# Performance work log

Measured on AMD Instinct MI355X. Metric: run time of the kernel, lower is better.

The kernel has to match this reference:

```python
import jax, jax.numpy as jnp
import numpy as np

B, T, S, H, C, E, V, OOV = 8, 16, 400, 512, 512, 128, 50000, 50


def setup_inputs() -> dict:
    key = jax.random.key(0)
    ks = jax.random.split(key, 24)
    rn = lambda k, shape, s=0.05: jax.random.normal(k, shape, dtype=jnp.float32) * s
    inp = {
        'input_embeddings': rn(ks[0], (B, T, E), 1.0),
        'context': rn(ks[1], (B, 1, C), 1.0),
        'h0': rn(ks[2], (1, B, H), 1.0),
        'c0': rn(ks[3], (1, B, H), 1.0),
        'encoder_outputs': rn(ks[4], (B, S, C), 1.0),
        'encoder_masks': jnp.ones((B, S), jnp.float32),
        'extra_zeros': jnp.zeros((B, OOV), jnp.float32),
        'extended_source_idx': jax.random.randint(ks[5], (B, S), 0, V + OOV),
        'coverage': jnp.zeros((B, 1, S), jnp.float32),
        # LSTM (single layer), torch gate order i,f,g,o
        'W_ih': rn(ks[6], (4 * H, E)), 'W_hh': rn(ks[7], (4 * H, H)),
        'b_ih': rn(ks[8], (4 * H,)), 'b_hh': rn(ks[9], (4 * H,)),
        # attention (concat + coverage)
        'cov_w': rn(ks[10], (H, 1)),
        'energy_w': rn(ks[11], (H, H + C)), 'energy_b': rn(ks[12], (H,)),
        'v': jax.random.uniform(ks[13], (H,), jnp.float32),
        # projections
        'xctx_w': rn(ks[14], (E, E + C)), 'xctx_b': rn(ks[15], (E,)),
        'attnd_w': rn(ks[16], (H, H + C)), 'attnd_b': rn(ks[17], (H,)),
        'vocab_w': rn(ks[18], (V, H)), 'vocab_b': rn(ks[19], (V,)),
        'pgen_w': rn(ks[20], (1, C + H + E)), 'pgen_b': rn(ks[21], (1,)),
    }
    return inp


def reference(input_embeddings, context, h0, c0, encoder_outputs, encoder_masks,
              extra_zeros, extended_source_idx, coverage,
              W_ih, W_hh, b_ih, b_hh, cov_w, energy_w, energy_b, v,
              xctx_w, xctx_b, attnd_w, attnd_b, vocab_w, vocab_b, pgen_w, pgen_b):
    Bn = input_embeddings.shape[0]
    Sn = encoder_outputs.shape[1]
    bidx = jnp.arange(Bn)[:, None]

    def step(carry, emb_t):
        h, c, ctx, cov = carry  # [B,H],[B,H],[B,C],[B,S]
        x = jnp.concatenate([emb_t, ctx], -1) @ xctx_w.T + xctx_b  # [B,E]
        gates = x @ W_ih.T + b_ih + h @ W_hh.T + b_hh
        i, f, g, o = jnp.split(gates, 4, axis=-1)
        c_new = jax.nn.sigmoid(f) * c + jax.nn.sigmoid(i) * jnp.tanh(g)
        h_new = jax.nn.sigmoid(o) * jnp.tanh(c_new)  # [B,H]
        # concat-style Luong attention with coverage
        cov_proj = cov[..., None] * cov_w[:, 0]  # [B,S,H] (Linear(1,H) no bias)
        cat = jnp.concatenate([
            jnp.broadcast_to(h_new[:, None, :], (Bn, Sn, h_new.shape[-1])),
            encoder_outputs], -1)  # [B,S,H+C]
        energy = jnp.tanh(cat @ energy_w.T + energy_b + cov_proj)
        e = energy @ v  # [B,S]
        probs = jax.nn.softmax(e, -1) * encoder_masks
        probs = probs / (probs.sum(-1, keepdims=True) + 1e-12)
        ctx_new = jnp.einsum('bs,bsc->bc', probs, encoder_outputs)
        cov_new = cov + probs
        vocab_dist = jax.nn.softmax(
            (jnp.concatenate([h_new, ctx_new], -1) @ attnd_w.T + attnd_b) @ vocab_w.T + vocab_b, -1)
        p_gen = jax.nn.sigmoid(jnp.concatenate([ctx_new, h_new, x], -1) @ pgen_w.T + pgen_b)  # [B,1]
        ext = jnp.concatenate([vocab_dist * p_gen, extra_zeros], 1)  # [B,V+OOV]
        final = ext.at[bidx, extended_source_idx].add((1.0 - p_gen) * probs)
        return (h_new, c_new, ctx_new, cov_new), (final, probs, cov_new, p_gen)

    init = (h0[0], c0[0], context[:, 0], coverage[:, 0])
    (h, c, ctx, cov), (finals, attns, covs, pgens) = jax.lax.scan(
        step, init, jnp.swapaxes(input_embeddings, 0, 1))
    final_vocab_dists = jnp.swapaxes(finals, 0, 1)  # [B,T,V+OOV]
    attn_dists = jnp.swapaxes(attns, 0, 1)          # [B,T,S]
    coverages = jnp.swapaxes(covs, 0, 1)            # [B,T,S]
    return (final_vocab_dists, ctx[:, None, :], h[None], c[None], attn_dists, pgens[-1], coverages)
```

## Files before the change

### kernel.cpp

```cpp
#include <hip/hip_runtime.h>
#include <math.h>

#define BB 8
#define TT 16
#define SS 400
#define HH 512
#define EE 128
#define VV 50000
#define VE 50050
#define OOVn 50

#define O1 6406400
#define O2 6410496
#define O3 6414592
#define O4 6418688
#define O5 6469888
#define O6 6469896

#define G_OFF    0
#define EWHB_OFF 1179648
#define ENCP_OFF 4600000
#define PM_OFF   5700000
#define CTXR_OFF 5800000

typedef __attribute__((ext_vector_type(4))) float floatx4;
typedef __attribute__((ext_vector_type(8))) short short8;
typedef __attribute__((ext_vector_type(8))) unsigned short ushort8_t;
typedef __attribute__((ext_vector_type(4))) unsigned short ushort4_t;

__device__ __forceinline__ float sigm(float x){ return 1.0f/(1.0f+__expf(-x)); }
__device__ __forceinline__ float ftanh(float x){
  float e = __expf(2.0f*x); return 1.0f - 2.0f/(e + 1.0f);
}
__device__ __forceinline__ unsigned short f2bf(float f){
  union { float f; unsigned int u; } v; v.f = f;
  unsigned int u = v.u;
  return (unsigned short)((u + 0x7FFFu + ((u >> 16) & 1u)) >> 16);
}
__device__ __forceinline__ float bfu(unsigned short u){
  union { unsigned int i; float f; } v; v.i = ((unsigned int)u) << 16; return v.f;
}

__global__ __launch_bounds__(256)
void gemm_bt(const float* __restrict__ A, int lda,
             const float* __restrict__ Bm, int ldb,
             const float* __restrict__ bias,
             float* __restrict__ Cm, int ldc,
             int N, int K, int permute, int obf,
             long bsB, long bsC)
{
  __shared__ unsigned short Ash[128*72];
  __shared__ unsigned short Bsh[64*72];
  int tid = threadIdx.x;
  int mbase = blockIdx.x * 128;
  int nbase = blockIdx.y * 64;
  long z = blockIdx.z;
  const float* Bz = Bm + z*bsB;
  int wave = tid >> 6, lane = tid & 63;
  int wm = (wave & 1) * 64, wn = (wave >> 1) * 32;
  int fl = lane & 15, quad = lane >> 4;

  floatx4 acc[4][2];
  for (int i=0;i<4;i++) for(int j=0;j<2;j++) acc[i][j] = (floatx4)(0.0f);

  for (int kc = 0; kc < K; kc += 64) {
    float4 ra[8], rb[4];
#pragma unroll
    for (int i = 0; i < 8; ++i) {
      int idx = tid + i*256;
      int row = idx >> 4;
      int c4 = (idx & 15) << 2;
      ra[i] = *(const float4*)(A + (size_t)(mbase+row)*lda + kc + c4);
    }
#pragma unroll
    for (int i = 0; i < 4; ++i) {
      int idx = tid + i*256;
      int row = idx >> 4;
      int c4 = (idx & 15) << 2;
      int gn = nbase + row;
      if (gn < N) rb[i] = *(const float4*)(Bz + (size_t)gn*ldb + kc + c4);
      else { rb[i].x = 0.f; rb[i].y = 0.f; rb[i].z = 0.f; rb[i].w = 0.f; }
    }
    __syncthreads();
#pragma unroll
    for (int i = 0; i < 8; ++i) {
      int idx = tid + i*256;
      int o = (idx >> 4)*72 + ((idx & 15) << 2);
      Ash[o+0]=f2bf(ra[i].x); Ash[o+1]=f2bf(ra[i].y); Ash[o+2]=f2bf(ra[i].z); Ash[o+3]=f2bf(ra[i].w);
    }
#pragma unroll
    for (int i = 0; i < 4; ++i) {
      int idx = tid + i*256;
      int o = (idx >> 4)*72 + ((idx & 15) << 2);
      Bsh[o+0]=f2bf(rb[i].x); Bsh[o+1]=f2bf(rb[i].y); Bsh[o+2]=f2bf(rb[i].z); Bsh[o+3]=f2bf(rb[i].w);
    }
    __syncthreads();
#pragma unroll
    for (int ks = 0; ks < 2; ++ks) {
      short8 af[4], bfr[2];
      int ko = ks*32 + quad*8;
#pragma unroll
      for (int i=0;i<4;i++) af[i]  = *(const short8*)&Ash[(wm + i*16 + fl)*72 + ko];
#pragma unroll
      for (int j=0;j<2;j++) bfr[j] = *(const short8*)&Bsh[(wn + j*16 + fl)*72 + ko];
#pragma unroll
      for (int i=0;i<4;i++)
#pragma unroll
        for (int j=0;j<2;j++)
          acc[i][j] = __builtin_amdgcn_mfma_f32_16x16x32_bf16(af[i], bfr[j], acc[i][j], 0,0,0);
    }
    __syncthreads();
  }
  for (int i=0;i<4;i++){
    for (int j=0;j<2;j++){
      int nc = nbase + wn + j*16 + fl;
      if (nc >= N) continue;
      float bv = bias ? bias[nc] : 0.0f;
      for (int r=0;r<4;r++){
        int mg = mbase + wm + i*16 + quad*4 + r;
        int orow = permute ? ((mg & 7)*16 + (mg >> 3)) : mg;
        float v = acc[i][j][r] + bv;
        long ci = (long)orow*ldc + nc + z*bsC;
        if (obf) ((unsigned short*)Cm)[ci] = f2bf(v);
        else     Cm[ci] = v;
      }
    }
  }
}

__global__ __launch_bounds__(256)
void gemm_logits(const unsigned short* __restrict__ Abf,
                 const float* __restrict__ Bm, const float* __restrict__ bias,
                 float* __restrict__ out, float* __restrict__ rowsum)
{
  __shared__ unsigned short Ash[128*72];
  __shared__ unsigned short Bsh[64*72];
  __shared__ float rowpart[128];
  int tid = threadIdx.x;
  int nbase = blockIdx.x * 64;
  int wave = tid >> 6, lane = tid & 63;
  int wm = (wave & 1) * 64, wn = (wave >> 1) * 32;
  int fl = lane & 15, quad = lane >> 4;

  floatx4 acc[4][2];
  for (int i=0;i<4;i++) for(int j=0;j<2;j++) acc[i][j] = (floatx4)(0.0f);
  if (tid < 128) rowpart[tid] = 0.f;

  for (int kc = 0; kc < 512; kc += 64) {
    ushort8_t raa[4];
    float4 rb[4];
#pragma unroll
    for (int i = 0; i < 4; ++i) {
      int idx = tid + i*256;
      int row = idx >> 3;
      int c8 = (idx & 7) << 3;
      raa[i] = *(const ushort8_t*)(Abf + (size_t)row*512 + kc + c8);
    }
#pragma unroll
    for (int i = 0; i < 4; ++i) {
      int idx = tid + i*256;
      int row = idx >> 4;
      int c4 = (idx & 15) << 2;
      int gn = nbase + row;
      if (gn < VV) rb[i] = *(const float4*)(Bm + (size_t)gn*512 + kc + c4);
      else { rb[i].x = 0.f; rb[i].y = 0.f; rb[i].z = 0.f; rb[i].w = 0.f; }
    }
    __syncthreads();
#pragma unroll
    for (int i = 0; i < 4; ++i) {
      int idx = tid + i*256;
      int o = (idx >> 3)*72 + ((idx & 7) << 3);
      *(ushort8_t*)&Ash[o] = raa[i];
    }
#pragma unroll
    for (int i = 0; i < 4; ++i) {
      int idx = tid + i*256;
      int o = (idx >> 4)*72 + ((idx & 15) << 2);
      Bsh[o+0]=f2bf(rb[i].x); Bsh[o+1]=f2bf(rb[i].y); Bsh[o+2]=f2bf(rb[i].z); Bsh[o+3]=f2bf(rb[i].w);
    }
    __syncthreads();
#pragma unroll
    for (int ks = 0; ks < 2; ++ks) {
      short8 af[4], bfr[2];
      int ko = ks*32 + quad*8;
#pragma unroll
      for (int i=0;i<4;i++) af[i]  = *(const short8*)&Ash[(wm + i*16 + fl)*72 + ko];
#pragma unroll
      for (int j=0;j<2;j++) bfr[j] = *(const short8*)&Bsh[(wn + j*16 + fl)*72 + ko];
#pragma unroll
      for (int i=0;i<4;i++)
#pragma unroll
        for (int j=0;j<2;j++)
          acc[i][j] = __builtin_amdgcn_mfma_f32_16x16x32_bf16(af[i], bfr[j], acc[i][j], 0,0,0);
    }
    __syncthreads();
  }
  for (int i=0;i<4;i++){
    for (int r=0;r<4;r++){
      int mg = wm + i*16 + quad*4 + r;
      int orow = (mg & 7)*16 + (mg >> 3);
      float rs = 0.f;
      for (int j=0;j<2;j++){
        int nc = nbase + wn + j*16 + fl;
        if (nc < VV) {
          float e = __expf(acc[i][j][r] + bias[nc]);
          out[(size_t)orow*VE + nc] = e;
          rs += e;
        }
      }
      atomicAdd(&rowpart[mg], rs);
    }
  }
  __syncthreads();
  if (tid < 128) {
    int orow = (tid & 7)*16 + (tid >> 3);
    atomicAdd(&rowsum[orow], rowpart[tid]);
  }
}

__global__ __launch_bounds__(256) void p_wx(const float* __restrict__ wih,
    const float* __restrict__ whh, const float* __restrict__ xcw,
    unsigned short* __restrict__ G)
{
  int blk = blockIdx.x, tid = threadIdx.x;
  if (blk < 640) {
    int rt = blk / 10, ct = blk % 10;
    __shared__ float wl[32*128];
    __shared__ float xl[128*64];
    for (int i = tid; i < 4096; i += 256) {
      int r = i >> 7, k = i & 127;
      wl[i] = wih[(size_t)(rt*32+r)*128 + k];
    }
    for (int i = tid; i < 8192; i += 256) {
      int e = i >> 6, c = i & 63;
      xl[i] = xcw[(size_t)e*640 + ct*64 + c];
    }
    __syncthreads();
    for (int o = tid; o < 2048; o += 256) {
      int r = o >> 6, c = o & 63;
      float acc = 0.f;
      for (int e = 0; e < 128; ++e) acc += wl[r*128+e]*xl[e*64+c];
      G[(size_t)(rt*32+r)*1152 + ct*64 + c] = f2bf(acc);
    }
  } else {
    int idx = blk - 640;
    for (int q = 0; q < 2; ++q) {
      int n = idx*2048 + q*1024 + tid*4;
      int r = n >> 9, k = n & 511;
      float4 v = *(const float4*)(whh + n);
      ushort4_t s; s[0]=f2bf(v.x); s[1]=f2bf(v.y); s[2]=f2bf(v.z); s[3]=f2bf(v.w);
      *(ushort4_t*)(G + (size_t)r*1152 + 640 + k) = s;
    }
  }
}

__global__ __launch_bounds__(256) void p_small(const float* __restrict__ wih,
    const float* __restrict__ bih, const float* __restrict__ bhh,
    const float* __restrict__ xb, const float* __restrict__ xcw,
    const float* __restrict__ pw, const float* __restrict__ pb,
    float* __restrict__ gb, float* __restrict__ q, float* __restrict__ qb,
    float* __restrict__ d1, float* __restrict__ d2)
{
  int blk = blockIdx.x, tid = threadIdx.x;
  if (blk < 8) {
    __shared__ float xbl[128];
    if (tid < 128) xbl[tid] = xb[tid];
    __syncthreads();
    int r = blk*256 + tid;
    const float* wr = wih + (size_t)r*128;
    float acc = bih[r] + bhh[r];
    for (int e = 0; e < 128; ++e) acc += wr[e]*xbl[e];
    gb[r] = acc;
  } else if (blk < 11) {
    int o = (blk-8)*256 + tid;
    if (o < 640) {
      float acc = 0.f;
      for (int e = 0; e < 128; ++e) acc += pw[1024+e]*xcw[(size_t)e*640 + o];
      q[o] = acc;
    }
  } else {
    if (tid == 0) {
      float acc = 0.f;
      for (int e = 0; e < 128; ++e) acc += pw[1024+e]*xb[e];
      qb[0] = acc + pb[0];
    }
    if (tid < 128) { d1[tid] = 0.f; d2[tid] = 0.f; }
  }
}

__global__ __launch_bounds__(256) void p_cast(const float* __restrict__ ew,
    unsigned short* __restrict__ ewhb, float* __restrict__ ctxraw)
{
  int blk = blockIdx.x, tid = threadIdx.x;
  for (int q = 0; q < 2; ++q) {
    size_t n = (size_t)blk*2048 + q*1024 + tid*4;
    int p = (int)(n >> 9), k = (int)(n & 511);
    float4 v = *(const float4*)(ew + (size_t)p*1024 + k);
    ushort4_t s; s[0]=f2bf(v.x); s[1]=f2bf(v.y); s[2]=f2bf(v.z); s[3]=f2bf(v.w);
    *(ushort4_t*)(ewhb + n) = s;
  }
  for (int i = tid; i < 512; i += 256) ctxraw[(size_t)blk*512 + i] = 0.f;
}

__global__ __launch_bounds__(256) void s1g(
    const unsigned short* __restrict__ G,
    const float* __restrict__ gb,
    const float* __restrict__ emb, const float* __restrict__ context,
    const float* __restrict__ h0, const float* __restrict__ c0,
    const float* __restrict__ coverage,
    const float* __restrict__ PM, const float* __restrict__ d1,
    const float* __restrict__ d2, const float* __restrict__ ctxraw,
    float* __restrict__ A1, float* __restrict__ c_cur,
    float* __restrict__ out, int t)
{
  __shared__ float ueh[8][644];
  __shared__ float uc[8][516];
  __shared__ float part[256];
  __shared__ float gl[64];
  __shared__ float invs[8];
  int tid = threadIdx.x, blk = blockIdx.x;

  if (t >= 1 && tid < 8)
    invs[tid] = 1.0f / (d2[(t-1)*8 + tid] + 1e-12f*d1[(t-1)*8 + tid]);
  __syncthreads();

  for (int i = 0; i < 5; ++i) {
    int slot = i*256 + tid;
    int b = slot / 160, sl = slot - b*160;
    if (sl < 32) {
      *(float4*)&ueh[b][sl*4] = *(const float4*)(emb + (size_t)(b*16+t)*128 + sl*4);
    } else {
      int qq = sl - 32;
      const float* hsrc = t ? (A1 + ((size_t)((t-1)*8+b))*1024) : (h0 + b*512);
      *(float4*)&ueh[b][128 + qq*4] = *(const float4*)(hsrc + qq*4);
    }
  }
  for (int i = 0; i < 4; ++i) {
    int slot = i*256 + tid;
    int b = slot >> 7, sl = slot & 127;
    const float* csrc = t ? (ctxraw + ((size_t)((t-1)*8+b))*512)
                          : (context + (size_t)b*512);
    float4 v = *(const float4*)(csrc + sl*4);
    if (t) { float iv = invs[b]; v.x*=iv; v.y*=iv; v.z*=iv; v.w*=iv; }
    *(float4*)&uc[b][sl*4] = v;
  }
  __syncthreads();

  if (t >= 1 && blk < 8) {
    int b = blk;
    float iv = invs[b];
    const float* covprev = (t == 1) ? (coverage + b*400)
                                    : (out + O6 + ((size_t)(b*16 + t-2))*400);
    const float* pmsrc = PM + (size_t)(t-1)*3200 + b*400;
    size_t o = ((size_t)(b*16 + t-1))*400;
    for (int s = tid; s < 400; s += 256) {
      float pr = pmsrc[s] * iv;
      out[O4 + o + s] = pr;
      out[O6 + o + s] = covprev[s] + pr;
    }
  }

  int dot = tid >> 2, kq = tid & 3;
  int rr = dot >> 3, b = dot & 7;
  int gate = rr >> 1, jj = rr & 1;
  int r = gate*512 + blk*2 + jj;
  const unsigned short* gr = G + (size_t)r*1152;
  float acc = 0.f;
  {
    const unsigned short* gp = gr + kq*8;
    const float* up = &ueh[b][kq*8];
#pragma unroll
    for (int i = 0; i < 4; ++i) {
      ushort8_t w8 = *(const ushort8_t*)(gp + i*32);
      float4 u0 = *(const float4*)(up + i*32);
      float4 u1 = *(const float4*)(up + i*32 + 4);
      acc += bfu(w8[0])*u0.x + bfu(w8[1])*u0.y + bfu(w8[2])*u0.z + bfu(w8[3])*u0.w
           + bfu(w8[4])*u1.x + bfu(w8[5])*u1.y + bfu(w8[6])*u1.z + bfu(w8[7])*u1.w;
    }
  }
  {
    const unsigned short* gp = gr + 128 + kq*8;
    const float* up = &uc[b][kq*8];
#pragma unroll 4
    for (int i = 0; i < 16; ++i) {
      ushort8_t w8 = *(const ushort8_t*)(gp + i*32);
      float4 u0 = *(const float4*)(up + i*32);
      float4 u1 = *(const float4*)(up + i*32 + 4);
      acc += bfu(w8[0])*u0.x + bfu(w8[1])*u0.y + bfu(w8[2])*u0.z + bfu(w8[3])*u0.w
           + bfu(w8[4])*u1.x + bfu(w8[5])*u1.y + bfu(w8[6])*u1.z + bfu(w8[7])*u1.w;
    }
  }
  {
    const unsigned short* gp = gr + 640 + kq*8;
    const float* up = &ueh[b][128 + kq*8];
#pragma unroll 4
    for (int i = 0; i < 16; ++i) {
      ushort8_t w8 = *(const ushort8_t*)(gp + i*32);
      float4 u0 = *(const float4*)(up + i*32);
      float4 u1 = *(const float4*)(up + i*32 + 4);
      acc += bfu(w8[0])*u0.x + bfu(w8[1])*u0.y + bfu(w8[2])*u0.z + bfu(w8[3])*u0.w
           + bfu(w8[4])*u1.x + bfu(w8[5])*u1.y + bfu(w8[6])*u1.z + bfu(w8[7])*u1.w;
    }
  }
  part[tid] = acc;
  __syncthreads();
  if (tid < 64) {
    int rr2 = tid >> 3;
    int r2 = (rr2 >> 1)*512 + blk*2 + (rr2 & 1);
    gl[tid] = part[tid*4] + part[tid*4+1] + part[tid*4+2] + part[tid*4+3] + gb[r2];
  }
  __syncthreads();
  if (tid < 16) {
    int jj2 = tid >> 3, b2 = tid & 7;
    float gi = gl[(0*2+jj2)*8 + b2];
    float gf = gl[(1*2+jj2)*8 + b2];
    float gg = gl[(2*2+jj2)*8 + b2];
    float go = gl[(3*2+jj2)*8 + b2];
    int j = blk*2 + jj2;
    float cp = t ? c_cur[b2*512+j] : c0[b2*512+j];
    float cn = sigm(gf)*cp + sigm(gi)*ftanh(gg);
    float hn = sigm(go)*ftanh(cn);
    c_cur[b2*512+j] = cn;
    A1[((size_t)(t*8+b2))*1024 + j] = hn;
  }
}

__global__ __launch_bounds__(256) void s2_hp(
    const unsigned short* __restrict__ ewhb, const float* __restrict__ eb,
    const float* __restrict__ A1, float* __restrict__ hp, int t)
{
  __shared__ float hl[8*516];
  __shared__ float part[256];
  int tid = threadIdx.x, pc = blockIdx.x;
  for (int b = 0; b < 8; ++b)
    for (int k = tid; k < 512; k += 256)
      hl[b*516 + k] = A1[((size_t)(t*8+b))*1024 + k];
  __syncthreads();
  int dot = tid >> 2, kq = tid & 3;
  int rr = dot >> 3, b = dot & 7;
  int p = pc*8 + rr;
  const unsigned short* wp = ewhb + (size_t)p*512 + kq*16;
  const float* hh = hl + b*516 + kq*16;
  float acc = 0.f;
#pragma unroll
  for (int i = 0; i < 8; ++i) {
    ushort8_t wa = *(const ushort8_t*)(wp + i*64);
    ushort8_t wb = *(const ushort8_t*)(wp + i*64 + 8);
    float4 h0v = *(const float4*)(hh + i*64);
    float4 h1v = *(const float4*)(hh + i*64 + 4);
    float4 h2v = *(const float4*)(hh + i*64 + 8);
    float4 h3v = *(const float4*)(hh + i*64 + 12);
    acc += bfu(wa[0])*h0v.x + bfu(wa[1])*h0v.y + bfu(wa[2])*h0v.z + bfu(wa[3])*h0v.w
         + bfu(wa[4])*h1v.x + bfu(wa[5])*h1v.y + bfu(wa[6])*h1v.z + bfu(wa[7])*h1v.w
         + bfu(wb[0])*h2v.x + bfu(wb[1])*h2v.y + bfu(wb[2])*h2v.z + bfu(wb[3])*h2v.w
         + bfu(wb[4])*h3v.x + bfu(wb[5])*h3v.y + bfu(wb[6])*h3v.z + bfu(wb[7])*h3v.w;
  }
  part[tid] = acc;
  __syncthreads();
  if (tid < 64) {
    int rr2 = tid >> 3, b2 = tid & 7;
    int p2 = pc*8 + rr2;
    hp[b2*512 + p2] = eb[p2] + part[tid*4] + part[tid*4+1] + part[tid*4+2] + part[tid*4+3];
  }
}

__global__ __launch_bounds__(256) void s3e(
    const unsigned short* __restrict__ encpb, const float* __restrict__ hp,
    const float* __restrict__ vvec, const float* __restrict__ covw,
    const float* __restrict__ masks, const float* __restrict__ coverage,
    const float* __restrict__ out6v, const float* __restrict__ enc,
    float* __restrict__ PM, float* __restrict__ d1, float* __restrict__ d2,
    float* __restrict__ ctxraw, int t)
{
  int tid = threadIdx.x;
  int b = blockIdx.x >> 4, sc = blockIdx.x & 15;
  int w = tid >> 6, lane = tid & 63;
  int h0i = lane*8;
  __shared__ float red1[4], red2[4];
  __shared__ float pms[25];
  float hpv[8], vv[8], cw[8];
  {
    const float* hpp = hp + b*512 + h0i;
    float4 a0 = *(const float4*)(hpp), a1 = *(const float4*)(hpp+4);
    hpv[0]=a0.x; hpv[1]=a0.y; hpv[2]=a0.z; hpv[3]=a0.w;
    hpv[4]=a1.x; hpv[5]=a1.y; hpv[6]=a1.z; hpv[7]=a1.w;
    float4 v0 = *(const float4*)(vvec+h0i), v1 = *(const float4*)(vvec+h0i+4);
    vv[0]=v0.x; vv[1]=v0.y; vv[2]=v0.z; vv[3]=v0.w;
    vv[4]=v1.x; vv[5]=v1.y; vv[6]=v1.z; vv[7]=v1.w;
    float4 c0v = *(const float4*)(covw+h0i), c1v = *(const float4*)(covw+h0i+4);
    cw[0]=c0v.x; cw[1]=c0v.y; cw[2]=c0v.z; cw[3]=c0v.w;
    cw[4]=c1v.x; cw[5]=c1v.y; cw[6]=c1v.z; cw[7]=c1v.w;
  }
  const float* covp = t ? (out6v + ((size_t)(b*16 + t-1))*400) : (coverage + b*400);
  float a1s = 0.f, a2s = 0.f;
  for (int sl = w; sl < 25; sl += 4) {
    int s = sc*25 + sl;
    float cv = covp[s];
    const unsigned short* ep = encpb + ((size_t)(b*400+s))*512 + h0i;
    ushort8_t e8 = *(const ushort8_t*)ep;
    float acc = 0.f;
#pragma unroll
    for (int i = 0; i < 8; ++i)
      acc += ftanh(hpv[i] + bfu(e8[i]) + cv*cw[i]) * vv[i];
    for (int off = 32; off > 0; off >>= 1) acc += __shfl_down(acc, off);
    if (lane == 0) {
      float pe = __expf(acc);
      float pmv = pe * masks[b*400 + s];
      PM[(size_t)t*3200 + b*400 + s] = pmv;
      pms[sl] = pmv;
      a1s += pe; a2s += pmv;
    }
  }
  if (lane == 0) { red1[w] = a1s; red2[w] = a2s; }
  __syncthreads();
  if (tid == 0) {
    atomicAdd(&d1[t*8+b], red1[0]+red1[1]+red1[2]+red1[3]);
    atomicAdd(&d2[t*8+b], red2[0]+red2[1]+red2[2]+red2[3]);
  }
  {
    float acc0 = 0.f, acc1 = 0.f;
    const float* encb = enc + ((size_t)(b*400 + sc*25))*512;
#pragma unroll 5
    for (int sl = 0; sl < 25; ++sl) {
      float pmv = pms[sl];
      const float* er = encb + (size_t)sl*512;
      acc0 += pmv * er[tid];
      acc1 += pmv * er[tid + 256];
    }
    float* cr = ctxraw + ((size_t)(t*8+b))*512;
    atomicAdd(&cr[tid], acc0);
    atomicAdd(&cr[tid+256], acc1);
  }
}

__global__ __launch_bounds__(256) void e_pgen(
    const float* __restrict__ A1f, const float* __restrict__ c_cur,
    const float* __restrict__ emb, const float* __restrict__ context,
    const float* __restrict__ pw, const float* __restrict__ q,
    const float* __restrict__ qb,
    const float* __restrict__ d1, const float* __restrict__ d2,
    const float* __restrict__ ctxraw, const float* __restrict__ PM,
    float* __restrict__ A1, float* __restrict__ pgen,
    float* __restrict__ rowsum, float* __restrict__ out)
{
  int blk = blockIdx.x, tid = threadIdx.x;
  if (blk < 128) {
    int m = blk, t = m >> 3, b = m & 7;
    __shared__ float invT, invP;
    if (tid == 0) invT = 1.0f / (d2[m] + 1e-12f*d1[m]);
    if (tid == 64) invP = t ? 1.0f / (d2[m-8] + 1e-12f*d1[m-8]) : 0.f;
    __syncthreads();
    const float* crT = ctxraw + (size_t)m*512;
    const float* crP = ctxraw + (size_t)(t ? m-8 : m)*512;
    const float* hT   = A1f + (size_t)m*1024;
    const float* embp = emb + (size_t)(b*16+t)*128;
    float acc = 0.f;
    for (int k = tid; k < 512; k += 256) {
      float cT = crT[k] * invT;
      float cP = t ? crP[k] * invP : context[(size_t)b*512 + k];
      acc += pw[k]*cT + pw[512+k]*hT[k] + q[128+k]*cP;
      A1[(size_t)m*1024 + 512 + k] = cT;
    }
    if (tid < 128) acc += q[tid]*embp[tid];
    for (int off = 32; off > 0; off >>= 1) acc += __shfl_down(acc, off);
    __shared__ float red[4];
    if (!(tid & 63)) red[tid>>6] = acc;
    __syncthreads();
    if (tid == 0) {
      float pg = sigm(red[0]+red[1]+red[2]+red[3] + qb[0]);
      pgen[m] = pg;
      if (t == 15) out[O5 + b] = pg;
    }
  } else if (blk == 128) {
    for (int i = tid; i < 4096; i += 256) {
      int b = i >> 9, j = i & 511;
      float inv = 1.0f / (d2[120+b] + 1e-12f*d1[120+b]);
      out[O1 + i] = ctxraw[(size_t)(120+b)*512 + j] * inv;
    }
  } else if (blk == 129) {
    for (int i = tid; i < 4096; i += 256) {
      int b = i >> 9, j = i & 511;
      out[O2 + i] = A1f[((size_t)(120+b))*1024 + j];
    }
  } else if (blk == 130) {
    for (int i = tid; i < 4096; i += 256) out[O3 + i] = c_cur[i];
  } else if (blk == 131) {
    if (tid < 128) rowsum[tid] = 0.f;
  } else {
    int b = blk - 132;
    float inv = 1.0f / (d2[120+b] + 1e-12f*d1[120+b]);
    const float* pmsrc = PM + (size_t)15*3200 + b*400;
    size_t o15 = ((size_t)(b*16 + 15))*400;
    size_t o14 = ((size_t)(b*16 + 14))*400;
    for (int s = tid; s < 400; s += 256) {
      float pr = pmsrc[s] * inv;
      out[O4 + o15 + s] = pr;
      out[O6 + o15 + s] = out[O6 + o14 + s] + pr;
    }
  }
}

__global__ __launch_bounds__(256) void k_scale(
    float* __restrict__ out, const float* __restrict__ pgen,
    const float* __restrict__ rowsum, const float* __restrict__ ez)
{
  int orow = blockIdx.x, cy = blockIdx.y, tid = threadIdx.x;
  int b = orow >> 4, t = orow & 15;
  float sc = pgen[t*8+b] / rowsum[orow];
  int c0 = cy*6256;
  int c1 = (cy == 7) ? VE : c0 + 6256;
  float* row = out + (size_t)orow*VE;
  for (int c = c0 + tid*4; c < c1; c += 1024) {
    if (c + 4 <= VV && c + 4 <= c1) {
      float4 v = *(float4*)(row + c);
      v.x *= sc; v.y *= sc; v.z *= sc; v.w *= sc;
      *(float4*)(row + c) = v;
    } else {
      for (int e = 0; e < 4; ++e) {
        int cc2 = c + e;
        if (cc2 < c1) row[cc2] = (cc2 < VV) ? row[cc2]*sc : ez[b*OOVn + cc2 - VV];
      }
    }
  }
}

__global__ __launch_bounds__(256) void k_scatter(
    float* __restrict__ out, const float* __restrict__ pgen,
    const int* __restrict__ extidx)
{
  int m = blockIdx.x, tid = threadIdx.x;
  int b = m & 7, t = m >> 3;
  float* row = out + ((size_t)(b*TT + t))*VE;
  float onem = 1.0f - pgen[m];
  const float* pr = out + O4 + ((size_t)(b*TT+t))*SS;
  for (int s = tid; s < SS; s += 256) {
    int ix = extidx[b*SS + s];
    atomicAdd(&row[ix], onem * pr[s]);
  }
}

extern "C" void kernel_launch(void* const* d_in, const int* in_sizes, int n_in,
                              void* d_out, int out_size, void* d_ws, size_t ws_size,
                              hipStream_t stream)
{
  (void)in_sizes; (void)n_in; (void)out_size; (void)ws_size;
  const float* emb      = (const float*)d_in[0];
  const float* context  = (const float*)d_in[1];
  const float* h0       = (const float*)d_in[2];
  const float* c0       = (const float*)d_in[3];
  const float* enc      = (const float*)d_in[4];
  const float* masks    = (const float*)d_in[5];
  const float* ez       = (const float*)d_in[6];
  const int*   extidx   = (const int*)d_in[7];
  const float* coverage = (const float*)d_in[8];
  const float* wih      = (const float*)d_in[9];
  const float* whh      = (const float*)d_in[10];
  const float* bih      = (const float*)d_in[11];
  const float* bhh      = (const float*)d_in[12];
  const float* covw     = (const float*)d_in[13];
  const float* ew       = (const float*)d_in[14];
  const float* eb       = (const float*)d_in[15];
  const float* vvec     = (const float*)d_in[16];
  const float* xw       = (const float*)d_in[17];
  const float* xb       = (const float*)d_in[18];
  const float* aw       = (const float*)d_in[19];
  const float* ab       = (const float*)d_in[20];
  const float* vw       = (const float*)d_in[21];
  const float* vb       = (const float*)d_in[22];
  const float* pw       = (const float*)d_in[23];
  const float* pb       = (const float*)d_in[24];
  float* out = (float*)d_out;

  float* ws = (float*)d_ws;
  float* A1       = ws;
  float* c_cur    = ws + 131072;
  float* hp       = ws + 135168;
  unsigned short* attnd_bf = (unsigned short*)(ws + 139264);
  float* pgen     = ws + 172032;
  float* gb       = ws + 172160;
  float* q        = ws + 174208;
  float* qb       = ws + 174848;
  float* d1       = ws + 174852;
  float* d2       = ws + 174980;
  float* rowsum   = ws + 175108;

  unsigned short* G     = (unsigned short*)(out + G_OFF);
  unsigned short* ewhb  = (unsigned short*)(out + EWHB_OFF);
  unsigned short* encpb = (unsigned short*)(out + ENCP_OFF);
  float*          PM    = out + PM_OFF;
  float*          ctxr  = out + CTXR_OFF;

  p_wx<<<1152, 256, 0, stream>>>(wih, whh, xw, G);
  p_small<<<12, 256, 0, stream>>>(wih, bih, bhh, xb, xw, pw, pb, gb, q, qb, d1, d2);
  p_cast<<<128, 256, 0, stream>>>(ew, ewhb, ctxr);
  gemm_bt<<<dim3(25,8,1), 256, 0, stream>>>(enc, 512, ew + 512, 1024,
      (const float*)nullptr, (float*)encpb, 512, 512, 512, 0, 1, 0, 0);

  for (int t = 0; t < TT; ++t) {
    s1g<<<256, 256, 0, stream>>>(G, gb, emb, context, h0, c0, coverage,
                                 PM, d1, d2, ctxr, A1, c_cur, out, t);
    s2_hp<<<64, 256, 0, stream>>>(ewhb, eb, A1, hp, t);
    s3e<<<128, 256, 0, stream>>>(encpb, hp, vvec, covw, masks, coverage,
                                 out + O6, enc, PM, d1, d2, ctxr, t);
  }

  e_pgen<<<140, 256, 0, stream>>>(A1, c_cur, emb, context, pw, q, qb,
                                  d1, d2, ctxr, PM, A1, pgen, rowsum, out);
  gemm_bt<<<dim3(1,8,1), 256, 0, stream>>>(A1, 1024, aw, 1024, ab,
      (float*)attnd_bf, 512, 512, 1024, 0, 1, 0, 0);
  gemm_logits<<<782, 256, 0, stream>>>(attnd_bf, vw, vb, out, rowsum);
  k_scale<<<dim3(128,8), 256, 0, stream>>>(out, pgen, rowsum, ez);
  k_scatter<<<128, 256, 0, stream>>>(out, pgen, extidx);
}
```

Before: 771.9 us.

## Fuse hidden-state energy projection into attention kernel, dropping per-step launch

Removes the separate s2_hp kernel that computed the hidden-state part of the attention energy, hp = energy_w_h·h + b. Each s3e block now recomputes the full 512-row projection for its own batch row, using a wave shuffle reduction, and keeps the result in shared memory. This cuts one kernel launch and one global round trip per timestep, 16 in total. In exchange, the 16 blocks that share a batch row each redo the same 512x512 bf16 matvec, so weight reads and compute go up 16x for that stage.

Result: slower. 796.7 us (+3.2%).

```diff
diff --git a/kernel.cpp b/kernel.cpp
--- a/kernel.cpp
+++ b/kernel.cpp
@@ -39,6 +39,13 @@
 }
 __device__ __forceinline__ float bfu(unsigned short u){
   union { unsigned int i; float f; } v; v.i = ((unsigned int)u) << 16; return v.f;
+}
+__device__ __forceinline__ float mac8(const unsigned short* w, const float* u) {
+  ushort8_t w8 = *(const ushort8_t*)w;
+  float4 u0 = *(const float4*)u;
+  float4 u1 = *(const float4*)(u+4);
+  return bfu(w8[0])*u0.x + bfu(w8[1])*u0.y + bfu(w8[2])*u0.z + bfu(w8[3])*u0.w
+       + bfu(w8[4])*u1.x + bfu(w8[5])*u1.y + bfu(w8[6])*u1.z + bfu(w8[7])*u1.w;
 }
 
 __global__ __launch_bounds__(256)
@@ -370,37 +377,19 @@
     const unsigned short* gp = gr + kq*8;
     const float* up = &ueh[b][kq*8];
 #pragma unroll
-    for (int i = 0; i < 4; ++i) {
-      ushort8_t w8 = *(const ushort8_t*)(gp + i*32);
-      float4 u0 = *(const float4*)(up + i*32);
-      float4 u1 = *(const float4*)(up + i*32 + 4);
-      acc += bfu(w8[0])*u0.x + bfu(w8[1])*u0.y + bfu(w8[2])*u0.z + bfu(w8[3])*u0.w
-           + bfu(w8[4])*u1.x + bfu(w8[5])*u1.y + bfu(w8[6])*u1.z + bfu(w8[7])*u1.w;
-    }
+    for (int i = 0; i < 4; ++i) acc += mac8(gp + i*32, up + i*32);
   }
   {
     const unsigned short* gp = gr + 128 + kq*8;
     const float* up = &uc[b][kq*8];
 #pragma unroll 4
-    for (int i = 0; i < 16; ++i) {
-      ushort8_t w8 = *(const ushort8_t*)(gp + i*32);
-      float4 u0 = *(const float4*)(up + i*32);
-      float4 u1 = *(const float4*)(up + i*32 + 4);
-      acc += bfu(w8[0])*u0.x + bfu(w8[1])*u0.y + bfu(w8[2])*u0.z + bfu(w8[3])*u0.w
-           + bfu(w8[4])*u1.x + bfu(w8[5])*u1.y + bfu(w8[6])*u1.z + bfu(w8[7])*u1.w;
-    }
+    for (int i = 0; i < 16; ++i) acc += mac8(gp + i*32, up + i*32);
   }
   {
     const unsigned short* gp = gr + 640 + kq*8;
     const float* up = &ueh[b][128 + kq*8];
 #pragma unroll 4
-    for (int i = 0; i < 16; ++i) {
-      ushort8_t w8 = *(const ushort8_t*)(gp + i*32);
-      float4 u0 = *(const float4*)(up + i*32);
-      float4 u1 = *(const float4*)(up + i*32 + 4);
-      acc += bfu(w8[0])*u0.x + bfu(w8[1])*u0.y + bfu(w8[2])*u0.z + bfu(w8[3])*u0.w
-           + bfu(w8[4])*u1.x + bfu(w8[5])*u1.y + bfu(w8[6])*u1.z + bfu(w8[7])*u1.w;
-    }
+    for (int i = 0; i < 16; ++i) acc += mac8(gp + i*32, up + i*32);
   }
   part[tid] = acc;
   __syncthreads();
@@ -425,47 +414,10 @@
   }
 }
 
-__global__ __launch_bounds__(256) void s2_hp(
-    const unsigned short* __restrict__ ewhb, const float* __restrict__ eb,
-    const float* __restrict__ A1, float* __restrict__ hp, int t)
-{
-  __shared__ float hl[8*516];
-  __shared__ float part[256];
-  int tid = threadIdx.x, pc = blockIdx.x;
-  for (int b = 0; b < 8; ++b)
-    for (int k = tid; k < 512; k += 256)
-      hl[b*516 + k] = A1[((size_t)(t*8+b))*1024 + k];
-  __syncthreads();
-  int dot = tid >> 2, kq = tid & 3;
-  int rr = dot >> 3, b = dot & 7;
-  int p = pc*8 + rr;
-  const unsigned short* wp = ewhb + (size_t)p*512 + kq*16;
-  const float* hh = hl + b*516 + kq*16;
-  float acc = 0.f;
-#pragma unroll
-  for (int i = 0; i < 8; ++i) {
-    ushort8_t wa = *(const ushort8_t*)(wp + i*64);
-    ushort8_t wb = *(const ushort8_t*)(wp + i*64 + 8);
-    float4 h0v = *(const float4*)(hh + i*64);
-    float4 h1v = *(const float4*)(hh + i*64 + 4);
-    float4 h2v = *(const float4*)(hh + i*64 + 8);
-    float4 h3v = *(const float4*)(hh + i*64 + 12);
-    acc += bfu(wa[0])*h0v.x + bfu(wa[1])*h0v.y + bfu(wa[2])*h0v.z + bfu(wa[3])*h0v.w
-         + bfu(wa[4])*h1v.x + bfu(wa[5])*h1v.y + bfu(wa[6])*h1v.z + bfu(wa[7])*h1v.w
-         + bfu(wb[0])*h2v.x + bfu(wb[1])*h2v.y + bfu(wb[2])*h2v.z + bfu(wb[3])*h2v.w
-         + bfu(wb[4])*h3v.x + bfu(wb[5])*h3v.y + bfu(wb[6])*h3v.z + bfu(wb[7])*h3v.w;
-  }
-  part[tid] = acc;
-  __syncthreads();
-  if (tid < 64) {
-    int rr2 = tid >> 3, b2 = tid & 7;
-    int p2 = pc*8 + rr2;
-    hp[b2*512 + p2] = eb[p2] + part[tid*4] + part[tid*4+1] + part[tid*4+2] + part[tid*4+3];
-  }
-}
-
 __global__ __launch_bounds__(256) void s3e(
-    const unsigned short* __restrict__ encpb, const float* __restrict__ hp,
+    const unsigned short* __restrict__ encpb,
+    const unsigned short* __restrict__ ewhb,
+    const float* __restrict__ eb, const float* __restrict__ A1,
     const float* __restrict__ vvec, const float* __restrict__ covw,
     const float* __restrict__ masks, const float* __restrict__ coverage,
     const float* __restrict__ out6v, const float* __restrict__ enc,
@@ -474,16 +426,41 @@
 {
   int tid = threadIdx.x;
   int b = blockIdx.x >> 4, sc = blockIdx.x & 15;
+  __shared__ float hl[512];
+  __shared__ float hpl[512];
+  __shared__ float red1[4], red2[4];
+  __shared__ float pms[25];
+
+  if (tid < 128)
+    *(float4*)&hl[tid*4] = *(const float4*)(A1 + ((size_t)(t*8+b))*1024 + tid*4);
+  __syncthreads();
+
+  {
+    int dot = tid >> 2, kq = tid & 3;
+    const float* hh = hl + kq*16;
+#pragma unroll
+    for (int pass = 0; pass < 8; ++pass) {
+      int p = pass*64 + dot;
+      const unsigned short* wp = ewhb + (size_t)p*512 + kq*16;
+      float acc = 0.f;
+#pragma unroll
+      for (int i = 0; i < 8; ++i) {
+        acc += mac8(wp + i*64, hh + i*64);
+        acc += mac8(wp + i*64 + 8, hh + i*64 + 8);
+      }
+      acc += __shfl_down(acc, 1);
+      acc += __shfl_down(acc, 2);
+      if (kq == 0) hpl[p] = eb[p] + acc;
+    }
+  }
+  __syncthreads();
+
   int w = tid >> 6, lane = tid & 63;
   int h0i = lane*8;
-  __shared__ float red1[4], red2[4];
-  __shared__ float pms[25];
   float hpv[8], vv[8], cw[8];
   {
-    const float* hpp = hp + b*512 + h0i;
-    float4 a0 = *(const float4*)(hpp), a1 = *(const float4*)(hpp+4);
-    hpv[0]=a0.x; hpv[1]=a0.y; hpv[2]=a0.z; hpv[3]=a0.w;
-    hpv[4]=a1.x; hpv[5]=a1.y; hpv[6]=a1.z; hpv[7]=a1.w;
+#pragma unroll
+    for (int i = 0; i < 8; ++i) hpv[i] = hpl[h0i + i];
     float4 v0 = *(const float4*)(vvec+h0i), v1 = *(const float4*)(vvec+h0i+4);
     vv[0]=v0.x; vv[1]=v0.y; vv[2]=v0.z; vv[3]=v0.w;
     vv[4]=v1.x; vv[5]=v1.y; vv[6]=v1.z; vv[7]=v1.w;
@@ -674,7 +651,6 @@
   float* ws = (float*)d_ws;
   float* A1       = ws;
   float* c_cur    = ws + 131072;
-  float* hp       = ws + 135168;
   unsigned short* attnd_bf = (unsigned short*)(ws + 139264);
   float* pgen     = ws + 172032;
   float* gb       = ws + 172160;
@@ -699,9 +675,8 @@
   for (int t = 0; t < TT; ++t) {
     s1g<<<256, 256, 0, stream>>>(G, gb, emb, context, h0, c0, coverage,
                                  PM, d1, d2, ctxr, A1, c_cur, out, t);
-    s2_hp<<<64, 256, 0, stream>>>(ewhb, eb, A1, hp, t);
-    s3e<<<128, 256, 0, stream>>>(encpb, hp, vvec, covw, masks, coverage,
-                                 out + O6, enc, PM, d1, d2, ctxr, t);
+    s3e<<<128, 256, 0, stream>>>(encpb, ewhb, eb, A1, vvec, covw, masks,
+                                 coverage, out + O6, enc, PM, d1, d2, ctxr, t);
   }
 
   e_pgen<<<140, 256, 0, stream>>>(A1, c_cur, emb, context, pw, q, qb,
```

## Replace 8-block attnd GEMM with wide GEMV kernel and fuse scatter into scale

Applied to the files above, without the earlier changes.

The attnd projection weights are now cast to bf16 in the existing prep cast kernel. The 8-block tiled GEMM is replaced with a 1024-block GEMV-style kernel in which each block reduces 8 output features for 8 rows, so a previously badly underfilled launch spreads across the GPU. The pointer-generator scatter is folded into the scale kernel: each column slice adds its own in-range indices after scaling, which removes one launch. The costs are an extra weight-cast pass and each scale block rereading the attention probabilities and indices.

Result: faster. 746.2 us (-3.3%).

```diff
diff --git a/kernel.cpp b/kernel.cpp
--- a/kernel.cpp
+++ b/kernel.cpp
@@ -19,6 +19,7 @@
 
 #define G_OFF    0
 #define EWHB_OFF 1179648
+#define AWBF_OFF 1310720
 #define ENCP_OFF 4600000
 #define PM_OFF   5700000
 #define CTXR_OFF 5800000
@@ -39,6 +40,13 @@
 }
 __device__ __forceinline__ float bfu(unsigned short u){
   union { unsigned int i; float f; } v; v.i = ((unsigned int)u) << 16; return v.f;
+}
+__device__ __forceinline__ float mac8(const unsigned short* w, const float* u) {
+  ushort8_t w8 = *(const ushort8_t*)w;
+  float4 u0 = *(const float4*)u;
+  float4 u1 = *(const float4*)(u+4);
+  return bfu(w8[0])*u0.x + bfu(w8[1])*u0.y + bfu(w8[2])*u0.z + bfu(w8[3])*u0.w
+       + bfu(w8[4])*u1.x + bfu(w8[5])*u1.y + bfu(w8[6])*u1.z + bfu(w8[7])*u1.w;
 }
 
 __global__ __launch_bounds__(256)
@@ -218,6 +226,41 @@
   }
 }
 
+__global__ __launch_bounds__(256) void vk_attnd(
+    const float* __restrict__ A1, const unsigned short* __restrict__ awbf,
+    const float* __restrict__ ab, unsigned short* __restrict__ attnd_bf)
+{
+  __shared__ float hl[8][1032];
+  __shared__ float part[256];
+  int tid = threadIdx.x;
+  int pc = blockIdx.x & 63;
+  int mg = blockIdx.x >> 6;
+  int m0 = mg*8;
+#pragma unroll
+  for (int i = 0; i < 8; ++i)
+    *(float4*)&hl[i][tid*4] = *(const float4*)(A1 + (size_t)(m0+i)*1024 + tid*4);
+  __syncthreads();
+  int dot = tid >> 2, kq = tid & 3;
+  int lp = dot >> 3, lm = dot & 7;
+  int p = pc*8 + lp;
+  const unsigned short* wp = awbf + (size_t)p*1024 + kq*16;
+  const float* hh = &hl[lm][kq*16];
+  float acc = 0.f;
+#pragma unroll
+  for (int i = 0; i < 16; ++i) {
+    acc += mac8(wp + i*64, hh + i*64);
+    acc += mac8(wp + i*64 + 8, hh + i*64 + 8);
+  }
+  part[tid] = acc;
+  __syncthreads();
+  if (tid < 64) {
+    int lp2 = tid >> 3, lm2 = tid & 7;
+    int p2 = pc*8 + lp2;
+    float v = ab[p2] + part[tid*4] + part[tid*4+1] + part[tid*4+2] + part[tid*4+3];
+    attnd_bf[(size_t)(m0+lm2)*512 + p2] = f2bf(v);
+  }
+}
+
 __global__ __launch_bounds__(256) void p_wx(const float* __restrict__ wih,
     const float* __restrict__ whh, const float* __restrict__ xcw,
     unsigned short* __restrict__ G)
@@ -289,17 +332,28 @@
 }
 
 __global__ __launch_bounds__(256) void p_cast(const float* __restrict__ ew,
-    unsigned short* __restrict__ ewhb, float* __restrict__ ctxraw)
+    unsigned short* __restrict__ ewhb, const float* __restrict__ aw,
+    unsigned short* __restrict__ awbf, float* __restrict__ ctxraw)
 {
   int blk = blockIdx.x, tid = threadIdx.x;
-  for (int q = 0; q < 2; ++q) {
-    size_t n = (size_t)blk*2048 + q*1024 + tid*4;
-    int p = (int)(n >> 9), k = (int)(n & 511);
-    float4 v = *(const float4*)(ew + (size_t)p*1024 + k);
-    ushort4_t s; s[0]=f2bf(v.x); s[1]=f2bf(v.y); s[2]=f2bf(v.z); s[3]=f2bf(v.w);
-    *(ushort4_t*)(ewhb + n) = s;
-  }
-  for (int i = tid; i < 512; i += 256) ctxraw[(size_t)blk*512 + i] = 0.f;
+  if (blk < 128) {
+    for (int q = 0; q < 2; ++q) {
+      size_t n = (size_t)blk*2048 + q*1024 + tid*4;
+      int p = (int)(n >> 9), k = (int)(n & 511);
+      float4 v = *(const float4*)(ew + (size_t)p*1024 + k);
+      ushort4_t s; s[0]=f2bf(v.x); s[1]=f2bf(v.y); s[2]=f2bf(v.z); s[3]=f2bf(v.w);
+      *(ushort4_t*)(ewhb + n) = s;
+    }
+    for (int i = tid; i < 512; i += 256) ctxraw[(size_t)blk*512 + i] = 0.f;
+  } else {
+    int idx = blk - 128;
+    for (int q = 0; q < 4; ++q) {
+      size_t n = (size_t)idx*4096 + q*1024 + tid*4;
+      float4 v = *(const float4*)(aw + n);
+      ushort4_t s; s[0]=f2bf(v.x); s[1]=f2bf(v.y); s[2]=f2bf(v.z); s[3]=f2bf(v.w);
+      *(ushort4_t*)(awbf + n) = s;
+    }
+  }
 }
 
 __global__ __launch_bounds__(256) void s1g(
@@ -370,37 +424,19 @@
     const unsigned short* gp = gr + kq*8;
     const float* up = &ueh[b][kq*8];
 #pragma unroll
-    for (int i = 0; i < 4; ++i) {
-      ushort8_t w8 = *(const ushort8_t*)(gp + i*32);
-      float4 u0 = *(const float4*)(up + i*32);
-      float4 u1 = *(const float4*)(up + i*32 + 4);
-      acc += bfu(w8[0])*u0.x + bfu(w8[1])*u0.y + bfu(w8[2])*u0.z + bfu(w8[3])*u0.w
-           + bfu(w8[4])*u1.x + bfu(w8[5])*u1.y + bfu(w8[6])*u1.z + bfu(w8[7])*u1.w;
-    }
+    for (int i = 0; i < 4; ++i) acc += mac8(gp + i*32, up + i*32);
   }
   {
     const unsigned short* gp = gr + 128 + kq*8;
     const float* up = &uc[b][kq*8];
 #pragma unroll 4
-    for (int i = 0; i < 16; ++i) {
-      ushort8_t w8 = *(const ushort8_t*)(gp + i*32);
-      float4 u0 = *(const float4*)(up + i*32);
-      float4 u1 = *(const float4*)(up + i*32 + 4);
-      acc += bfu(w8[0])*u0.x + bfu(w8[1])*u0.y + bfu(w8[2])*u0.z + bfu(w8[3])*u0.w
-           + bfu(w8[4])*u1.x + bfu(w8[5])*u1.y + bfu(w8[6])*u1.z + bfu(w8[7])*u1.w;
-    }
+    for (int i = 0; i < 16; ++i) acc += mac8(gp + i*32, up + i*32);
   }
   {
     const unsigned short* gp = gr + 640 + kq*8;
     const float* up = &ueh[b][128 + kq*8];
 #pragma unroll 4
-    for (int i = 0; i < 16; ++i) {
-      ushort8_t w8 = *(const ushort8_t*)(gp + i*32);
-      float4 u0 = *(const float4*)(up + i*32);
-      float4 u1 = *(const float4*)(up + i*32 + 4);
-      acc += bfu(w8[0])*u0.x + bfu(w8[1])*u0.y + bfu(w8[2])*u0.z + bfu(w8[3])*u0.w
-           + bfu(w8[4])*u1.x + bfu(w8[5])*u1.y + bfu(w8[6])*u1.z + bfu(w8[7])*u1.w;
-    }
+    for (int i = 0; i < 16; ++i) acc += mac8(gp + i*32, up + i*32);
   }
   part[tid] = acc;
   __syncthreads();
@@ -444,16 +480,8 @@
   float acc = 0.f;
 #pragma unroll
   for (int i = 0; i < 8; ++i) {
-    ushort8_t wa = *(const ushort8_t*)(wp + i*64);
-    ushort8_t wb = *(const ushort8_t*)(wp + i*64 + 8);
-    float4 h0v = *(const float4*)(hh + i*64);
-    float4 h1v = *(const float4*)(hh + i*64 + 4);
-    float4 h2v = *(const float4*)(hh + i*64 + 8);
-    float4 h3v = *(const float4*)(hh + i*64 + 12);
-    acc += bfu(wa[0])*h0v.x + bfu(wa[1])*h0v.y + bfu(wa[2])*h0v.z + bfu(wa[3])*h0v.w
-         + bfu(wa[4])*h1v.x + bfu(wa[5])*h1v.y + bfu(wa[6])*h1v.z + bfu(wa[7])*h1v.w
-         + bfu(wb[0])*h2v.x + bfu(wb[1])*h2v.y + bfu(wb[2])*h2v.z + bfu(wb[3])*h2v.w
-         + bfu(wb[4])*h3v.x + bfu(wb[5])*h3v.y + bfu(wb[6])*h3v.z + bfu(wb[7])*h3v.w;
+    acc += mac8(wp + i*64, hh + i*64);
+    acc += mac8(wp + i*64 + 8, hh + i*64 + 8);
   }
   part[tid] = acc;
   __syncthreads();
@@ -602,7 +630,8 @@
 
 __global__ __launch_bounds__(256) void k_scale(
     float* __restrict__ out, const float* __restrict__ pgen,
-    const float* __restrict__ rowsum, const float* __restrict__ ez)
+    const float* __restrict__ rowsum, const float* __restrict__ ez,
+    const int* __restrict__ extidx)
 {
   int orow = blockIdx.x, cy = blockIdx.y, tid = threadIdx.x;
   int b = orow >> 4, t = orow & 15;
@@ -622,20 +651,13 @@
       }
     }
   }
-}
-
-__global__ __launch_bounds__(256) void k_scatter(
-    float* __restrict__ out, const float* __restrict__ pgen,
-    const int* __restrict__ extidx)
-{
-  int m = blockIdx.x, tid = threadIdx.x;
-  int b = m & 7, t = m >> 3;
-  float* row = out + ((size_t)(b*TT + t))*VE;
-  float onem = 1.0f - pgen[m];
-  const float* pr = out + O4 + ((size_t)(b*TT+t))*SS;
+  __syncthreads();
+  float onem = 1.0f - pgen[t*8+b];
+  const float* pr = out + O4 + (size_t)orow*SS;
   for (int s = tid; s < SS; s += 256) {
     int ix = extidx[b*SS + s];
-    atomicAdd(&row[ix], onem * pr[s]);
+    if (ix >= c0 && ix < c1)
+      atomicAdd(&row[ix], onem * pr[s]);
   }
 }
 
@@ -686,13 +708,14 @@
 
   unsigned short* G     = (unsigned short*)(out + G_OFF);
   unsigned short* ewhb  = (unsigned short*)(out + EWHB_OFF);
+  unsigned short* awbf  = (unsigned short*)(out + AWBF_OFF);
   unsigned short* encpb = (unsigned short*)(out + ENCP_OFF);
   float*          PM    = out + PM_OFF;
   float*          ctxr  = out + CTXR_OFF;
 
   p_wx<<<1152, 256, 0, stream>>>(wih, whh, xw, G);
   p_small<<<12, 256, 0, stream>>>(wih, bih, bhh, xb, xw, pw, pb, gb, q, qb, d1, d2);
-  p_cast<<<128, 256, 0, stream>>>(ew, ewhb, ctxr);
+  p_cast<<<256, 256, 0, stream>>>(ew, ewhb, aw, awbf, ctxr);
   gemm_bt<<<dim3(25,8,1), 256, 0, stream>>>(enc, 512, ew + 512, 1024,
       (const float*)nullptr, (float*)encpb, 512, 512, 512, 0, 1, 0, 0);
 
@@ -706,9 +729,7 @@
 
   e_pgen<<<140, 256, 0, stream>>>(A1, c_cur, emb, context, pw, q, qb,
                                   d1, d2, ctxr, PM, A1, pgen, rowsum, out);
-  gemm_bt<<<dim3(1,8,1), 256, 0, stream>>>(A1, 1024, aw, 1024, ab,
-      (float*)attnd_bf, 512, 512, 1024, 0, 1, 0, 0);
+  vk_attnd<<<1024, 256, 0, stream>>>(A1, awbf, ab, attnd_bf);
   gemm_logits<<<782, 256, 0, stream>>>(attnd_bf, vw, vb, out, rowsum);
-  k_scale<<<dim3(128,8), 256, 0, stream>>>(out, pgen, rowsum, ez);
-  k_scatter<<<128, 256, 0, stream>>>(out, pgen, extidx);
-}
+  k_scale<<<dim3(128,8), 256, 0, stream>>>(out, pgen, rowsum, ez, extidx);
+}
```
